# Kernel optimization log

Measured on AMD Instinct MI355X. Metric: run time of the kernel, lower is better.

The kernel has to match this reference:

```python
import jax, jax.numpy as jnp
import numpy as np
import math

SR = 16000
WIN = 320
HOP = 160
NFFT = 512
NMEL = 64
PREEMPH = 0.97
LOG_GUARD = 2.0 ** (-24)
PAD_TO = 16
EPS = 1e-5  # CONSTANT added to std


def _slaney_mel_fbanks(sr=SR, n_fft=NFFT, n_mels=NMEL, fmin=0.0, fmax=8000.0):
    """Replicates torchaudio.functional.melscale_fbanks(norm='slaney', mel_scale='slaney').
    Returns [n_mels, n_freqs] (already transposed like the torch buffer `fb`)."""
    n_freqs = n_fft // 2 + 1
    all_freqs = np.linspace(0.0, sr / 2.0, n_freqs)
    f_sp = 200.0 / 3.0
    min_log_hz = 1000.0
    min_log_mel = min_log_hz / f_sp
    logstep = math.log(6.4) / 27.0

    def hz2mel(f):
        f = np.asarray(f, dtype=np.float64)
        return np.where(f >= min_log_hz,
                        min_log_mel + np.log(np.maximum(f, 1e-10) / min_log_hz) / logstep,
                        f / f_sp)

    def mel2hz(m):
        m = np.asarray(m, dtype=np.float64)
        return np.where(m >= min_log_mel,
                        min_log_hz * np.exp(logstep * (m - min_log_mel)),
                        f_sp * m)

    m_pts = np.linspace(hz2mel(fmin), hz2mel(fmax), n_mels + 2)
    f_pts = mel2hz(m_pts)                       # [n_mels+2]
    f_diff = f_pts[1:] - f_pts[:-1]             # [n_mels+1]
    slopes = f_pts[None, :] - all_freqs[:, None]  # [n_freqs, n_mels+2]
    down = -slopes[:, :-2] / f_diff[:-1]
    up = slopes[:, 2:] / f_diff[1:]
    fb = np.maximum(0.0, np.minimum(down, up))  # [n_freqs, n_mels]
    enorm = 2.0 / (f_pts[2:] - f_pts[:-2])      # slaney area normalization
    fb = fb * enorm[None, :]
    return fb.T.astype(np.float32)              # [n_mels, n_freqs]


def _hann_window_padded(win_length=WIN, n_fft=NFFT):
    # the window symmetrically to n_fft.
    w = np.hanning(win_length).astype(np.float32)
    left = (n_fft - win_length) // 2
    out = np.zeros(n_fft, dtype=np.float32)
    out[left:left + win_length] = w
    return out


def setup_inputs() -> dict:
    key = jax.random.key(0)
    kx, kl = jax.random.split(key)
    B, L = 32, 256000
    x = jax.random.normal(kx, (B, L), dtype=jnp.float32)
    # ragged valid lengths in [L/2, L] (plenty of frames per feature)
    seq_len = jax.random.randint(kl, (B,), L // 2, L + 1, dtype=jnp.int32)
    window = jnp.asarray(_hann_window_padded())       # [NFFT]
    fb = jnp.asarray(_slaney_mel_fbanks())            # [NMEL, NFFT//2+1]
    return {"x": x, "seq_len": seq_len, "window": window, "fb": fb}


def _forward(x, seq_len, window, fb):
    B, L = x.shape
    # get_seq_len: pad_amount = 2*(n_fft//2); floor((L + pad - n_fft)/hop) + 1
    feat_len = (seq_len + NFFT - NFFT) // HOP + 1     # = seq_len // HOP + 1
    # pre-emphasis
    x = jnp.concatenate([x[:, :1], x[:, 1:] - PREEMPH * x[:, :-1]], axis=1)
    # STFT, center=True reflect padding (eval mode: no dither)
    pad = NFFT // 2
    xp = jnp.pad(x, ((0, 0), (pad, pad)), mode='reflect')
    T = L // HOP + 1                                  # 1601 frames
    idx = jnp.arange(T)[:, None] * HOP + jnp.arange(NFFT)[None, :]
    frames = xp[:, idx] * window                      # [B, T, NFFT]
    spec = jnp.fft.rfft(frames, axis=-1)              # [B, T, F]
    # magnitude then mag_power=2 -> power spectrum (guard=0 since use_grads=False)
    pow_spec = spec.real ** 2 + spec.imag ** 2        # [B, T, F]
    mel = jnp.einsum('mf,btf->bmt', fb, pow_spec)     # [B, NMEL, T]
    logmel = jnp.log(mel + LOG_GUARD)
    # per_feature masked normalization (torch.std is unbiased -> /(n-1)), std += 1e-5
    mask = (jnp.arange(T)[None, :] < feat_len[:, None])          # [B, T]
    m = mask[:, None, :].astype(logmel.dtype)                    # [B, 1, T]
    n = feat_len.astype(logmel.dtype)[:, None, None]
    mean = jnp.sum(logmel * m, axis=2, keepdims=True) / n
    var = jnp.sum(((logmel - mean) * m) ** 2, axis=2, keepdims=True) / (n - 1.0)
    std = jnp.sqrt(var) + EPS
    out = (logmel - mean) / std
    # fill padding frames with pad_value=0
    out = jnp.where(m > 0, out, 0.0)
    # pad time dim to a multiple of pad_to=16 with pad_value
    pad_amt = (-T) % PAD_TO
    out = jnp.pad(out, ((0, 0), (0, 0), (0, pad_amt)), constant_values=0.0)
    return out, feat_len


def reference(x, seq_len, window, fb):
    return _forward(x, seq_len, window, fb)
```

## Files before the change

kernel.cpp:

```cpp
#include <hip/hip_runtime.h>
#include <math.h>

#define L_IN 256000
#define T_FR 1601
#define T_PAD 1616
#define NMEL_K 64
#define F_BINS 257
#define HOP_K 160
#define PRE_E 0.97f
#define LOG_GUARD_K 5.9604644775390625e-08f
#define FPB 16
#define CONC 4
#define GROUPS 101
#define SPAN 2912

__device__ __forceinline__ float2 cmulf(float2 a, float2 b) {
  return make_float2(a.x * b.x - a.y * b.y, a.x * b.y + a.y * b.x);
}

__device__ __forceinline__ float dpp_xor1(float x) {
  return __int_as_float(__builtin_amdgcn_mov_dpp(__float_as_int(x), 0xB1, 0xF, 0xF, true));
}
__device__ __forceinline__ float dpp_xor2(float x) {
  return __int_as_float(__builtin_amdgcn_mov_dpp(__float_as_int(x), 0x4E, 0xF, 0xF, true));
}

__device__ __forceinline__ double mel2hz_d(double mel, double logstep) {
  return (mel < 15.0) ? mel * (200.0 / 3.0) : 1000.0 * exp(logstep * (mel - 15.0));
}

#define FFT_STAGE(I, PR, PI)                                        \
  {                                                                 \
    const int H__ = 32 >> (I);                                      \
    const bool hi__ = (lane & H__) != 0;                            \
    const float cc__ = stc[I], ss__ = sts[I];                       \
    _Pragma("unroll")                                               \
    for (int r = 0; r < 4; ++r) {                                   \
      float tr = (PR), ti = (PI);                                   \
      float sr = Br[r] + tr, si = Bi[r] + ti;                       \
      float dr = tr - Br[r], di = ti - Bi[r];                       \
      float pr = dr * cc__ - di * ss__, pi = dr * ss__ + di * cc__; \
      Br[r] = hi__ ? pr : sr;                                       \
      Bi[r] = hi__ ? pi : si;                                       \
    }                                                               \
  }

__global__ void __launch_bounds__(256) frame_fft_mel_kernel(
    const float* __restrict__ x, const int* __restrict__ seq_len,
    const float* __restrict__ window, float* __restrict__ out,
    float* __restrict__ part) {
  __shared__ __align__(16) float xs[SPAN];
  __shared__ __align__(16) float pw[CONC][288];
  __shared__ float outm[NMEL_K][FPB + 1];

  const int tid = threadIdx.x;
  const int w = tid >> 6;
  const int lane = tid & 63;
  const int b = blockIdx.x / GROUPS;
  const int g = blockIdx.x - b * GROUPS;
  const int t0 = g * FPB;
  const float* xb = x + (size_t)b * L_IN;
  const int base = t0 * HOP_K - 256;
  const int fl = seq_len[b] / HOP_K + 1;

  if (base >= 0 && base + SPAN <= L_IN) {
    const float4* xb4 = (const float4*)(xb + base);
    float4* xs4 = (float4*)xs;
    for (int s4 = tid; s4 < SPAN / 4; s4 += 256) {
      float4 cur = xb4[s4];
      float prev = xb[base + 4 * s4 - 1];
      float4 o;
      o.x = fmaf(-PRE_E, prev, cur.x);
      o.y = fmaf(-PRE_E, cur.x, cur.y);
      o.z = fmaf(-PRE_E, cur.y, cur.z);
      o.w = fmaf(-PRE_E, cur.z, cur.w);
      xs4[s4] = o;
    }
  } else {
    for (int n = tid; n < SPAN; n += 256) {
      int i = base + n;
      i = (i < 0) ? -i : i;
      i = (i >= L_IN) ? (2 * L_IN - 2 - i) : i;
      xs[n] = (i == 0) ? xb[0] : fmaf(-PRE_E, xb[i - 1], xb[i]);
    }
  }

  if (lane >= 33 && lane < 64) pw[w][224 + lane] = 0.0f;

  int la;
  float fw[32];
  {
    const double logstep = log(6.4) / 27.0;
    const double mmax = 15.0 + log(8.0) / logstep;
    const double step = mmax / 65.0;
    double fp0 = mel2hz_d((double)lane * step, logstep);
    double fp1 = mel2hz_d((double)(lane + 1) * step, logstep);
    double fp2 = mel2hz_d((double)(lane + 2) * step, logstep);
    la = ((int)floor(fp0 / 31.25) + 1) & ~3;
    float f0f = (float)fp0, f2f = (float)fp2;
    float i01 = (float)(1.0 / (fp1 - fp0));
    float i12 = (float)(1.0 / (fp2 - fp1));
    float en = (float)(2.0 / (fp2 - fp0));
#pragma unroll
    for (int jj = 0; jj < 32; ++jj) {
      float fj = (float)(la + jj) * 31.25f;
      float v = fminf((fj - f0f) * i01, (f2f - fj) * i12);
      fw[jj] = fmaxf(0.0f, v) * en;
    }
  }

  const int sig = __builtin_bitreverse32(lane) >> 26;
  float wr[4], wi[4];
#pragma unroll
  for (int q = 0; q < 4; ++q) {
    float2 wv = *(const float2*)(window + 2 * (lane + 64 * q));
    wr[q] = wv.x; wi[q] = wv.y;
  }
  float2 tw1, tw2, tw3;
  {
    float a = -0.024543692606170259f * (float)lane;
    __sincosf(a, &tw1.y, &tw1.x);
    tw2 = cmulf(tw1, tw1);
    tw3 = cmulf(tw2, tw1);
  }
  float stc[6], sts[6];
#pragma unroll
  for (int i = 0; i < 6; ++i) {
    int H = 32 >> i;
    int p = lane & (H - 1);
    float a = -3.14159265358979323846f * (float)p / (float)H;
    __sincosf(a, &sts[i], &stc[i]);
  }
  float cu[4], su[4];
  {
    float a = -0.049087385212340519f * (float)sig;
    float cb, sb;
    __sincosf(a, &sb, &cb);
    const float C[4] = {1.0f, 0.99992470183914454f, 0.99969881869620425f, 0.99932238458834954f};
    const float S[4] = {0.0f, 0.01227153828571993f, 0.02454122852291229f, 0.03680722294135883f};
#pragma unroll
    for (int r = 0; r < 4; ++r) {
      cu[r] = cb * C[r] + sb * S[r];
      su[r] = sb * C[r] - cb * S[r];
    }
  }
  const int idx0 = __builtin_bitreverse32((64 - sig) & 63) >> 26;

  __syncthreads();

  float sm = 0.0f, ssq = 0.0f;

  for (int c = 0; c < FPB / CONC; ++c) {
    const int j = c * CONC + w;
    const int off = j * HOP_K;

    float Br[4], Bi[4];
    {
      float zr[4], zi[4];
#pragma unroll
      for (int q = 0; q < 4; ++q) {
        float2 v = *(const float2*)(xs + off + 2 * (lane + 64 * q));
        zr[q] = v.x * wr[q];
        zi[q] = v.y * wi[q];
      }
      float e0r = zr[0] + zr[2], e0i = zi[0] + zi[2];
      float e1r = zr[1] + zr[3], e1i = zi[1] + zi[3];
      float d0r = zr[0] - zr[2], d0i = zi[0] - zi[2];
      float d1r = zr[1] - zr[3], d1i = zi[1] - zi[3];
      Br[0] = e0r + e1r; Bi[0] = e0i + e1i;
      float A2r = e0r - e1r, A2i = e0i - e1i;
      float A1r = d0r + d1i, A1i = d0i - d1r;
      float A3r = d0r - d1i, A3i = d0i + d1r;
      Br[1] = A1r * tw1.x - A1i * tw1.y; Bi[1] = A1r * tw1.y + A1i * tw1.x;
      Br[2] = A2r * tw2.x - A2i * tw2.y; Bi[2] = A2r * tw2.y + A2i * tw2.x;
      Br[3] = A3r * tw3.x - A3i * tw3.y; Bi[3] = A3r * tw3.y + A3i * tw3.x;
    }

    FFT_STAGE(0, __shfl_xor(Br[r], 32), __shfl_xor(Bi[r], 32));
    FFT_STAGE(1, __shfl_xor(Br[r], 16), __shfl_xor(Bi[r], 16));
    FFT_STAGE(2, __shfl_xor(Br[r], 8), __shfl_xor(Bi[r], 8));
    FFT_STAGE(3, __shfl_xor(Br[r], 4), __shfl_xor(Bi[r], 4));
    FFT_STAGE(4, dpp_xor2(Br[r]), dpp_xor2(Bi[r]));
    FFT_STAGE(5, dpp_xor1(Br[r]), dpp_xor1(Bi[r]));

    {
      float q3r = __shfl_xor(Br[3], 63), q3i = __shfl_xor(Bi[3], 63);
      float q2r = __shfl_xor(Br[2], 63), q2i = __shfl_xor(Bi[2], 63);
      float q1r = __shfl_xor(Br[1], 63), q1i = __shfl_xor(Bi[1], 63);
      float q0r = __shfl(Br[0], idx0), q0i = __shfl(Bi[0], idx0);
      float qr[4] = {q0r, q3r, q2r, q1r};
      float qi_[4] = {q0i, q3i, q2i, q1i};
      float pv[4];
#pragma unroll
      for (int r = 0; r < 4; ++r) {
        float Er = 0.5f * (Br[r] + qr[r]);
        float Ei = 0.5f * (Bi[r] - qi_[r]);
        float Or = 0.5f * (Bi[r] + qi_[r]);
        float Oi = 0.5f * (qr[r] - Br[r]);
        float Xr = Er + cu[r] * Or - su[r] * Oi;
        float Xi = Ei + cu[r] * Oi + su[r] * Or;
        pv[r] = Xr * Xr + Xi * Xi;
      }
      ((float4*)pw[w])[sig] = make_float4(pv[0], pv[1], pv[2], pv[3]);
      if (lane == 0) { float d = Br[0] - Bi[0]; pw[w][256] = d * d; }
    }
    __builtin_amdgcn_wave_barrier();

    {
      const float4* pq = (const float4*)pw[w] + (la >> 2);
      float acc = 0.0f;
#pragma unroll
      for (int jj = 0; jj < 8; ++jj) {
        float4 p = pq[jj];
        acc = fmaf(fw[4 * jj], p.x, acc);
        acc = fmaf(fw[4 * jj + 1], p.y, acc);
        acc = fmaf(fw[4 * jj + 2], p.z, acc);
        acc = fmaf(fw[4 * jj + 3], p.w, acc);
      }
      float lv = __logf(acc + LOG_GUARD_K);
      outm[lane][j] = lv;
      if (t0 + j < fl) { sm += lv; ssq = fmaf(lv, lv, ssq); }
    }
    __builtin_amdgcn_wave_barrier();
  }

  pw[w][lane] = sm;
  pw[w][64 + lane] = ssq;

  __syncthreads();

#pragma unroll
  for (int p = 0; p < 4; ++p) {
    int row = p * 16 + (tid >> 4);
    int jj = tid & 15;
    int t = t0 + jj;
    if (t < T_FR)
      out[((size_t)(b << 6) + row) * T_PAD + t] = outm[row][jj];
  }

  if (tid < 64) {
    float s0 = pw[0][tid] + pw[1][tid] + pw[2][tid] + pw[3][tid];
    float q0 = pw[0][64 + tid] + pw[1][64 + tid] + pw[2][64 + tid] + pw[3][64 + tid];
    float* pp = part + (size_t)blockIdx.x * 128;
    pp[tid] = s0;
    pp[64 + tid] = q0;
  }
}

__global__ void __launch_bounds__(256) norm_kernel2(
    const int* __restrict__ seq_len, const float* __restrict__ part,
    float* __restrict__ out, float* __restrict__ fl_out) {
  const int bm = blockIdx.x;
  const int b = bm >> 6;
  const int m = bm & 63;
  const int tid = threadIdx.x;
  const int fl = seq_len[b] / HOP_K + 1;

  float ps = 0.0f, pq = 0.0f;
  for (int g = tid; g < GROUPS; g += 256) {
    const float* pp = part + (size_t)(b * GROUPS + g) * 128;
    ps += pp[m];
    pq += pp[64 + m];
  }
  __shared__ float red[8];
  __shared__ float bc[2];
#pragma unroll
  for (int off = 32; off > 0; off >>= 1) {
    ps += __shfl_down(ps, off, 64);
    pq += __shfl_down(pq, off, 64);
  }
  if ((tid & 63) == 0) { red[tid >> 6] = ps; red[4 + (tid >> 6)] = pq; }
  __syncthreads();
  if (tid == 0) {
    float s = red[0] + red[1] + red[2] + red[3];
    float q = red[4] + red[5] + red[6] + red[7];
    float n = (float)fl;
    float mean = s / n;
    float var = (q - s * mean) / (n - 1.0f);
    bc[0] = mean;
    bc[1] = 1.0f / (sqrtf(var) + 1e-5f);
  }
  __syncthreads();
  const float mean = bc[0], istd = bc[1];
  float4* rowp = (float4*)(out + (size_t)bm * T_PAD);
  for (int c4 = tid; c4 < T_PAD / 4; c4 += 256) {
    float4 v = rowp[c4];
    int t = 4 * c4;
    float4 o;
    o.x = (t < fl) ? (v.x - mean) * istd : 0.0f;
    o.y = (t + 1 < fl) ? (v.y - mean) * istd : 0.0f;
    o.z = (t + 2 < fl) ? (v.z - mean) * istd : 0.0f;
    o.w = (t + 3 < fl) ? (v.w - mean) * istd : 0.0f;
    rowp[c4] = o;
  }
  if (m == 0 && tid == 0) fl_out[b] = (float)fl;
}

extern "C" void kernel_launch(void* const* d_in, const int* in_sizes, int n_in,
                              void* d_out, int out_size, void* d_ws, size_t ws_size,
                              hipStream_t stream) {
  const float* x = (const float*)d_in[0];
  const int* seq_len = (const int*)d_in[1];
  const float* window = (const float*)d_in[2];
  float* out = (float*)d_out;
  float* fl_out = out + (size_t)32 * NMEL_K * T_PAD;
  float* part = (float*)d_ws;

  frame_fft_mel_kernel<<<32 * GROUPS, 256, 0, stream>>>(x, seq_len, window, out, part);
  norm_kernel2<<<32 * NMEL_K, 256, 0, stream>>>(seq_len, part, out, fl_out);
}
```

Baseline: 127.0 us.

## Halve frames per block and load mel weights from a compacted filterbank

Each block now covers 8 frames instead of 16, which doubles the grid and shrinks the shared-memory staging span, giving more blocks to spread across CUs. The per-thread double-precision mel filterbank computation is replaced by a small prep kernel that compacts the supplied fb input into 32-wide aligned windows per mel band, and the main kernel reads those weights from global memory. The cost is an extra launch, more overlap between neighbouring blocks' input spans (halo reloaded per block), and twice as many partial-sum rows for the norm kernel to reduce.

```diff
diff --git a/kernel.cpp b/kernel.cpp
--- a/kernel.cpp
+++ b/kernel.cpp
@@ -9,10 +9,10 @@
 #define HOP_K 160
 #define PRE_E 0.97f
 #define LOG_GUARD_K 5.9604644775390625e-08f
-#define FPB 16
+#define FPB 8
 #define CONC 4
-#define GROUPS 101
-#define SPAN 2912
+#define GROUPS 201
+#define SPAN 1632
 
 __device__ __forceinline__ float2 cmulf(float2 a, float2 b) {
   return make_float2(a.x * b.x - a.y * b.y, a.x * b.y + a.y * b.x);
@@ -25,8 +25,31 @@
   return __int_as_float(__builtin_amdgcn_mov_dpp(__float_as_int(x), 0x4E, 0xF, 0xF, true));
 }
 
-__device__ __forceinline__ double mel2hz_d(double mel, double logstep) {
-  return (mel < 15.0) ? mel * (200.0 / 3.0) : 1000.0 * exp(logstep * (mel - 15.0));
+__global__ void prep_kernel(const float* __restrict__ fb, float* __restrict__ fbc,
+                            int* __restrict__ loAl) {
+  const int m = blockIdx.x;
+  const int t = threadIdx.x;
+  int first = 512, last = -1;
+  for (int c = 0; c < 5; ++c) {
+    int f = t + 64 * c;
+    if (f < F_BINS) {
+      float v = fb[m * F_BINS + f];
+      if (v > 0.0f) { first = min(first, f); last = max(last, f); }
+    }
+  }
+  for (int off = 32; off > 0; off >>= 1) {
+    first = min(first, __shfl_xor(first, off));
+    last = max(last, __shfl_xor(last, off));
+  }
+  int lo = (first <= last) ? first : 0;
+  int lastv = (first <= last) ? last : 0;
+  int la = lo & ~3;
+  if (t == 0) loAl[m] = la;
+  if (t < 32) {
+    int f = la + t;
+    float v = (f >= lo && f <= lastv && f < F_BINS) ? fb[m * F_BINS + f] : 0.0f;
+    fbc[m * 32 + t] = v;
+  }
 }
 
 #define FFT_STAGE(I, PR, PI)                                        \
@@ -47,7 +70,8 @@
 
 __global__ void __launch_bounds__(256) frame_fft_mel_kernel(
     const float* __restrict__ x, const int* __restrict__ seq_len,
-    const float* __restrict__ window, float* __restrict__ out,
+    const float* __restrict__ window, const float* __restrict__ fbc,
+    const int* __restrict__ loAl, float* __restrict__ out,
     float* __restrict__ part) {
   __shared__ __align__(16) float xs[SPAN];
   __shared__ __align__(16) float pw[CONC][288];
@@ -87,28 +111,6 @@
 
   if (lane >= 33 && lane < 64) pw[w][224 + lane] = 0.0f;
 
-  int la;
-  float fw[32];
-  {
-    const double logstep = log(6.4) / 27.0;
-    const double mmax = 15.0 + log(8.0) / logstep;
-    const double step = mmax / 65.0;
-    double fp0 = mel2hz_d((double)lane * step, logstep);
-    double fp1 = mel2hz_d((double)(lane + 1) * step, logstep);
-    double fp2 = mel2hz_d((double)(lane + 2) * step, logstep);
-    la = ((int)floor(fp0 / 31.25) + 1) & ~3;
-    float f0f = (float)fp0, f2f = (float)fp2;
-    float i01 = (float)(1.0 / (fp1 - fp0));
-    float i12 = (float)(1.0 / (fp2 - fp1));
-    float en = (float)(2.0 / (fp2 - fp0));
-#pragma unroll
-    for (int jj = 0; jj < 32; ++jj) {
-      float fj = (float)(la + jj) * 31.25f;
-      float v = fminf((fj - f0f) * i01, (f2f - fj) * i12);
-      fw[jj] = fmaxf(0.0f, v) * en;
-    }
-  }
-
   const int sig = __builtin_bitreverse32(lane) >> 26;
   float wr[4], wi[4];
 #pragma unroll
@@ -145,6 +147,8 @@
     }
   }
   const int idx0 = __builtin_bitreverse32((64 - sig) & 63) >> 26;
+  const int la = loAl[lane];
+  const float4* fr4 = (const float4*)fbc + lane * 8;
 
   __syncthreads();
 
@@ -211,11 +215,12 @@
       float acc = 0.0f;
 #pragma unroll
       for (int jj = 0; jj < 8; ++jj) {
+        float4 wq = fr4[jj];
         float4 p = pq[jj];
-        acc = fmaf(fw[4 * jj], p.x, acc);
-        acc = fmaf(fw[4 * jj + 1], p.y, acc);
-        acc = fmaf(fw[4 * jj + 2], p.z, acc);
-        acc = fmaf(fw[4 * jj + 3], p.w, acc);
+        acc = fmaf(wq.x, p.x, acc);
+        acc = fmaf(wq.y, p.y, acc);
+        acc = fmaf(wq.z, p.z, acc);
+        acc = fmaf(wq.w, p.w, acc);
       }
       float lv = __logf(acc + LOG_GUARD_K);
       outm[lane][j] = lv;
@@ -230,9 +235,9 @@
   __syncthreads();
 
 #pragma unroll
-  for (int p = 0; p < 4; ++p) {
-    int row = p * 16 + (tid >> 4);
-    int jj = tid & 15;
+  for (int p = 0; p < 2; ++p) {
+    int row = p * 32 + (tid >> 3);
+    int jj = tid & 7;
     int t = t0 + jj;
     if (t < T_FR)
       out[((size_t)(b << 6) + row) * T_PAD + t] = outm[row][jj];
@@ -302,10 +307,15 @@
   const float* x = (const float*)d_in[0];
   const int* seq_len = (const int*)d_in[1];
   const float* window = (const float*)d_in[2];
+  const float* fb = (const float*)d_in[3];
   float* out = (float*)d_out;
   float* fl_out = out + (size_t)32 * NMEL_K * T_PAD;
   float* part = (float*)d_ws;
-
-  frame_fft_mel_kernel<<<32 * GROUPS, 256, 0, stream>>>(x, seq_len, window, out, part);
+  float* fbc = (float*)((char*)d_ws + (size_t)32 * GROUPS * 128 * 4);
+  int* loAl = (int*)((char*)d_ws + (size_t)32 * GROUPS * 128 * 4 + 8192);
+
+  prep_kernel<<<NMEL_K, 64, 0, stream>>>(fb, fbc, loAl);
+  frame_fft_mel_kernel<<<32 * GROUPS, 256, 0, stream>>>(x, seq_len, window, fbc,
+                                                        loAl, out, part);
   norm_kernel2<<<32 * NMEL_K, 256, 0, stream>>>(seq_len, part, out, fl_out);
 }
```

Result: slower. 145.2 us (+14.3%).
